# Optimization experiments

Hardware: AMD Instinct MI355X
Metric: run time of the kernel (lower is better)

Reference implementation:

```python
import jax, jax.numpy as jnp
import numpy as np


def setup_inputs() -> dict:
    key = jax.random.key(0)
    k1, k2, k3 = jax.random.split(key, 3)
    B, Na, Nb = 64, 8192, 8192
    phases_a = jax.random.normal(k1, (B, Na), dtype=jnp.float32)
    phases_b = jax.random.normal(k2, (B, Nb), dtype=jnp.float32)
    # Binary coupled-pair indicator mask (N_a, N_b)
    coupling_mask = jax.random.randint(k3, (Na, Nb), 0, 2, dtype=jnp.int32)
    return {"phases_a": phases_a, "phases_b": phases_b, "coupling_mask": coupling_mask}


def reference(phases_a, phases_b, coupling_mask):
    """Masked phase-locking value (PLV) between two oscillator banks.

    Mathematically identical to |sum_ij M_ij * exp(i*(a_i - b_j))| / sum(M),
    but computed via trig identities + matmul instead of materializing the
    O(B*Na*Nb) complex tensor:
      real = sum_ij M_ij (cos a_i cos b_j + sin a_i sin b_j)
      imag = sum_ij M_ij (sin a_i cos b_j - cos a_i sin b_j)
    """
    ca, sa = jnp.cos(phases_a), jnp.sin(phases_a)   # (B, Na)
    cb, sb = jnp.cos(phases_b), jnp.sin(phases_b)   # (B, Nb)
    M = coupling_mask.astype(ca.dtype)              # (Na, Nb)
    caM = ca @ M                                    # (B, Nb)
    saM = sa @ M                                    # (B, Nb)
    real = jnp.sum(caM * cb + saM * sb, axis=-1)    # (B,)
    imag = jnp.sum(saM * cb - caM * sb, axis=-1)    # (B,)
    n_pairs = jnp.maximum(M.sum(), jnp.asarray(1.0, ca.dtype))
    return jnp.sqrt(real * real + imag * imag) / n_pairs
```

## Files before the change

kernel.cpp:

```cpp
#include <hip/hip_runtime.h>
#include <hip/hip_bf16.h>

#define NA 8192
#define NB 8192
#define NBATCH 64
#define NC 128
#define BM 128
#define WM 32
#define SPLITK 8
#define KCHUNK (NB / SPLITK)

#define XT_BYTES (NC * NB * 2)
#define CTR_OFF  XT_BYTES
#define PPART_OFF (XT_BYTES + 4096)

typedef __bf16 bf16x8 __attribute__((ext_vector_type(8)));
typedef float  f32x4  __attribute__((ext_vector_type(4)));

__global__ __launch_bounds__(256) void prep_b_kernel(
    const float* __restrict__ pb, __hip_bfloat16* __restrict__ Xt)
{
    int tid = blockIdx.x * 256 + threadIdx.x;
    int b = tid >> 13;
    int j = tid & (NB - 1);
    float ph = pb[tid];
    float s, c;
    __sincosf(ph, &s, &c);
    Xt[(size_t)(2 * b) * NB + j]     = __float2bfloat16(c);
    Xt[(size_t)(2 * b + 1) * NB + j] = __float2bfloat16(s);
}

__global__ __launch_bounds__(256, 2) void gemm_kernel(
    const int* __restrict__ mask, const __hip_bfloat16* __restrict__ Xtg,
    float* __restrict__ Ppart, int* __restrict__ count)
{
    const int tid  = threadIdx.x;
    const int wave = tid >> 6;
    const int lane = tid & 63;
    const int quad = lane >> 4;
    const int m    = lane & 15;
    const int itile = blockIdx.x;
    const int kc    = blockIdx.y;
    const int k0    = kc * KCHUNK;

    const int rowbase = itile * BM + wave * WM;
    const ushort* xt = reinterpret_cast<const ushort*>(Xtg);

    f32x4 acc[2][8];
#pragma unroll
    for (int f = 0; f < 2; ++f)
#pragma unroll
        for (int t = 0; t < 8; ++t)
            acc[f][t] = (f32x4){0.f, 0.f, 0.f, 0.f};

    int cnt = 0;

    for (int kk = k0; kk < k0 + KCHUNK; kk += 32) {
        const int kq = kk + quad * 8;

        bf16x8 a[2];
#pragma unroll
        for (int f = 0; f < 2; ++f) {
            const int4* p = reinterpret_cast<const int4*>(
                mask + (size_t)(rowbase + f * 16 + m) * NB + kq);
            int4 r0 = p[0];
            int4 r1 = p[1];
            cnt += r0.x + r0.y + r0.z + r0.w + r1.x + r1.y + r1.z + r1.w;
            uint4 u;
            u.x = (r0.x ? 0x3F80u : 0u) | (r0.y ? 0x3F800000u : 0u);
            u.y = (r0.z ? 0x3F80u : 0u) | (r0.w ? 0x3F800000u : 0u);
            u.z = (r1.x ? 0x3F80u : 0u) | (r1.y ? 0x3F800000u : 0u);
            u.w = (r1.z ? 0x3F80u : 0u) | (r1.w ? 0x3F800000u : 0u);
            a[f] = __builtin_bit_cast(bf16x8, u);
        }

#pragma unroll
        for (int t = 0; t < 8; ++t) {
            const bf16x8 bfrag = *reinterpret_cast<const bf16x8*>(
                xt + (size_t)(t * 16 + m) * NB + kq);
            acc[0][t] = __builtin_amdgcn_mfma_f32_16x16x32_bf16(a[0], bfrag, acc[0][t], 0, 0, 0);
            acc[1][t] = __builtin_amdgcn_mfma_f32_16x16x32_bf16(a[1], bfrag, acc[1][t], 0, 0, 0);
        }
    }

    float* pout = Ppart + (size_t)kc * NA * NC;
#pragma unroll
    for (int f = 0; f < 2; ++f)
#pragma unroll
        for (int t = 0; t < 8; ++t)
#pragma unroll
            for (int r = 0; r < 4; ++r) {
                int row = rowbase + f * 16 + quad * 4 + r;
                int col = t * 16 + m;
                pout[(size_t)row * NC + col] = acc[f][t][r];
            }

#pragma unroll
    for (int off = 32; off > 0; off >>= 1) cnt += __shfl_down(cnt, off);
    if (lane == 0) atomicAdd(count, cnt);
}

__global__ __launch_bounds__(256) void reduce_kernel(
    const float* __restrict__ pa, const float* __restrict__ Ppart,
    float* __restrict__ realg, float* __restrict__ imagg)
{
    const int t = threadIdx.x;
    const int c = t & 127;
    const int half = t >> 7;
    const int b = c >> 1;
    const int odd = c & 1;
    const int i0 = blockIdx.x * 32;

    float pacc = 0.f, qacc = 0.f;
    for (int i = i0 + half; i < i0 + 32; i += 2) {
        float v = 0.f;
#pragma unroll
        for (int kc = 0; kc < SPLITK; ++kc)
            v += Ppart[(size_t)kc * NA * NC + (size_t)i * NC + c];
        float ph = pa[b * NA + i];
        float sn, cs;
        __sincosf(ph, &sn, &cs);
        float yc = odd ? sn : cs;
        float yo = odd ? cs : sn;
        pacc += yc * v;
        qacc += odd ? -(yo * v) : (yo * v);
    }

    __shared__ float red[2][256];
    red[0][t] = pacc;
    red[1][t] = qacc;
    __syncthreads();
    if (t < 128) {
        red[0][t] = red[0][t] + red[0][t + 128];
        red[1][t] = red[1][t] + red[1][t + 128];
    }
    __syncthreads();
    if (t < 64) {
        float real = red[0][2 * t] + red[0][2 * t + 1];
        float imag = red[1][2 * t] + red[1][2 * t + 1];
        atomicAdd(&realg[t], real);
        atomicAdd(&imagg[t], imag);
    }
}

__global__ void finalize_kernel(const float* __restrict__ realg,
                                const float* __restrict__ imagg,
                                const int* __restrict__ count,
                                float* __restrict__ out)
{
    int t = threadIdx.x;
    if (t < NBATCH) {
        float r = realg[t], im = imagg[t];
        float n = fmaxf((float)(*count), 1.0f);
        out[t] = sqrtf(r * r + im * im) / n;
    }
}

extern "C" void kernel_launch(void* const* d_in, const int* in_sizes, int n_in,
                              void* d_out, int out_size, void* d_ws, size_t ws_size,
                              hipStream_t stream) {
    const float* pa   = (const float*)d_in[0];
    const float* pb   = (const float*)d_in[1];
    const int*   mask = (const int*)d_in[2];
    float* out = (float*)d_out;

    char* ws = (char*)d_ws;
    __hip_bfloat16* Xt = (__hip_bfloat16*)ws;
    float* realg = (float*)(ws + CTR_OFF);
    float* imagg = realg + 64;
    int*   count = (int*)(ws + CTR_OFF + 512);
    float* Ppart = (float*)(ws + PPART_OFF);

    hipMemsetAsync(ws + CTR_OFF, 0, 4096, stream);

    prep_b_kernel<<<(NBATCH * NB) / 256, 256, 0, stream>>>(pb, Xt);

    dim3 g(NA / BM, SPLITK);
    gemm_kernel<<<g, 256, 0, stream>>>(mask, Xt, Ppart, count);

    reduce_kernel<<<NA / 32, 256, 0, stream>>>(pa, Ppart, realg, imagg);

    finalize_kernel<<<1, 64, 0, stream>>>(realg, imagg, count, out);
}
```

Measured before the change: 431.9 us.

## Compress int32 mask to bitmask before GEMM and permute B columns to match

```diff
diff --git a/kernel.cpp b/kernel.cpp
--- a/kernel.cpp
+++ b/kernel.cpp
@@ -9,30 +9,86 @@
 #define WM 32
 #define SPLITK 8
 #define KCHUNK (NB / SPLITK)
-
-#define XT_BYTES (NC * NB * 2)
-#define CTR_OFF  XT_BYTES
-#define PPART_OFF (XT_BYTES + 4096)
+#define NBW (NB / 32)
+
+#define XT_BYTES   (NC * NB * 2)
+#define BITS_OFF   XT_BYTES
+#define BITS_BYTES (NA * (NB / 8))
+#define CTR_OFF    (BITS_OFF + BITS_BYTES)
+#define PPART_OFF  (CTR_OFF + 4096)
 
 typedef __bf16 bf16x8 __attribute__((ext_vector_type(8)));
 typedef float  f32x4  __attribute__((ext_vector_type(4)));
 
+
+__global__ __launch_bounds__(256) void compress_kernel(
+    const int* __restrict__ mask, unsigned int* __restrict__ bits,
+    int* __restrict__ count)
+{
+    const int lane   = threadIdx.x & 63;
+    const int gwave  = (blockIdx.x * 256 + threadIdx.x) >> 6;
+    const int nwaves = (gridDim.x * 256) >> 6;
+
+    int cnt = 0;
+    const int total_iters = NA * (NB / 512);
+    for (int it = gwave; it < total_iters; it += nwaves) {
+        const int r  = it >> 4;
+        const int j0 = (it & 15) << 9;
+        const int4* p = reinterpret_cast<const int4*>(mask + (size_t)r * NB + j0);
+        int4 v0 = p[lane];
+        int4 v1 = p[lane + 64];
+
+        unsigned long long b0 = __ballot(v0.x != 0);
+        unsigned long long b1 = __ballot(v0.y != 0);
+        unsigned long long b2 = __ballot(v0.z != 0);
+        unsigned long long b3 = __ballot(v0.w != 0);
+        unsigned long long b4 = __ballot(v1.x != 0);
+        unsigned long long b5 = __ballot(v1.y != 0);
+        unsigned long long b6 = __ballot(v1.z != 0);
+        unsigned long long b7 = __ballot(v1.w != 0);
+
+        cnt += __builtin_popcountll(b0) + __builtin_popcountll(b1)
+             + __builtin_popcountll(b2) + __builtin_popcountll(b3)
+             + __builtin_popcountll(b4) + __builtin_popcountll(b5)
+             + __builtin_popcountll(b6) + __builtin_popcountll(b7);
+
+        if (lane == 0) {
+            uint4* o = reinterpret_cast<uint4*>(bits + (size_t)r * NBW + (j0 >> 5));
+            o[0] = (uint4){(unsigned)b0, (unsigned)(b0 >> 32), (unsigned)b1, (unsigned)(b1 >> 32)};
+            o[1] = (uint4){(unsigned)b2, (unsigned)(b2 >> 32), (unsigned)b3, (unsigned)(b3 >> 32)};
+            o[2] = (uint4){(unsigned)b4, (unsigned)(b4 >> 32), (unsigned)b5, (unsigned)(b5 >> 32)};
+            o[3] = (uint4){(unsigned)b6, (unsigned)(b6 >> 32), (unsigned)b7, (unsigned)(b7 >> 32)};
+        }
+    }
+    if (lane == 0) atomicAdd(count, cnt);
+}
+
 __global__ __launch_bounds__(256) void prep_b_kernel(
     const float* __restrict__ pb, __hip_bfloat16* __restrict__ Xt)
 {
     int tid = blockIdx.x * 256 + threadIdx.x;
-    int b = tid >> 13;
-    int j = tid & (NB - 1);
-    float ph = pb[tid];
+    int b  = tid >> 13;
+    int kp = tid & (NB - 1);
+    int j  = (kp & ~255) | ((kp & 63) << 2) | ((kp >> 6) & 3);
+    float ph = pb[(size_t)b * NB + j];
     float s, c;
     __sincosf(ph, &s, &c);
-    Xt[(size_t)(2 * b) * NB + j]     = __float2bfloat16(c);
-    Xt[(size_t)(2 * b + 1) * NB + j] = __float2bfloat16(s);
+    Xt[(size_t)(2 * b) * NB + kp]     = __float2bfloat16(c);
+    Xt[(size_t)(2 * b + 1) * NB + kp] = __float2bfloat16(s);
+}
+
+__device__ inline bf16x8 expand8(unsigned int byte) {
+    uint4 u;
+    u.x = ((((byte >> 1) & 1u) << 16) | (byte & 1u))          * 0x3F80u;
+    u.y = ((((byte >> 3) & 1u) << 16) | ((byte >> 2) & 1u))   * 0x3F80u;
+    u.z = ((((byte >> 5) & 1u) << 16) | ((byte >> 4) & 1u))   * 0x3F80u;
+    u.w = ((((byte >> 7) & 1u) << 16) | ((byte >> 6) & 1u))   * 0x3F80u;
+    return __builtin_bit_cast(bf16x8, u);
 }
 
 __global__ __launch_bounds__(256, 2) void gemm_kernel(
-    const int* __restrict__ mask, const __hip_bfloat16* __restrict__ Xtg,
-    float* __restrict__ Ppart, int* __restrict__ count)
+    const unsigned int* __restrict__ bits, const __hip_bfloat16* __restrict__ Xtg,
+    float* __restrict__ Ppart)
 {
     const int tid  = threadIdx.x;
     const int wave = tid >> 6;
@@ -45,6 +101,7 @@
 
     const int rowbase = itile * BM + wave * WM;
     const ushort* xt = reinterpret_cast<const ushort*>(Xtg);
+    const int qsh = quad * 8;
 
     f32x4 acc[2][8];
 #pragma unroll
@@ -53,33 +110,24 @@
         for (int t = 0; t < 8; ++t)
             acc[f][t] = (f32x4){0.f, 0.f, 0.f, 0.f};
 
-    int cnt = 0;
+    const unsigned int* w0p = bits + (size_t)(rowbase + m) * NBW;
+    const unsigned int* w1p = bits + (size_t)(rowbase + 16 + m) * NBW;
 
     for (int kk = k0; kk < k0 + KCHUNK; kk += 32) {
-        const int kq = kk + quad * 8;
-
-        bf16x8 a[2];
-#pragma unroll
-        for (int f = 0; f < 2; ++f) {
-            const int4* p = reinterpret_cast<const int4*>(
-                mask + (size_t)(rowbase + f * 16 + m) * NB + kq);
-            int4 r0 = p[0];
-            int4 r1 = p[1];
-            cnt += r0.x + r0.y + r0.z + r0.w + r1.x + r1.y + r1.z + r1.w;
-            uint4 u;
-            u.x = (r0.x ? 0x3F80u : 0u) | (r0.y ? 0x3F800000u : 0u);
-            u.y = (r0.z ? 0x3F80u : 0u) | (r0.w ? 0x3F800000u : 0u);
-            u.z = (r1.x ? 0x3F80u : 0u) | (r1.y ? 0x3F800000u : 0u);
-            u.w = (r1.z ? 0x3F80u : 0u) | (r1.w ? 0x3F800000u : 0u);
-            a[f] = __builtin_bit_cast(bf16x8, u);
-        }
+        const int wi = kk >> 5;
+        unsigned int w0 = w0p[wi];
+        unsigned int w1 = w1p[wi];
+        const int kq = kk + qsh;
+
+        bf16x8 a0 = expand8((w0 >> qsh) & 0xFFu);
+        bf16x8 a1 = expand8((w1 >> qsh) & 0xFFu);
 
 #pragma unroll
         for (int t = 0; t < 8; ++t) {
             const bf16x8 bfrag = *reinterpret_cast<const bf16x8*>(
                 xt + (size_t)(t * 16 + m) * NB + kq);
-            acc[0][t] = __builtin_amdgcn_mfma_f32_16x16x32_bf16(a[0], bfrag, acc[0][t], 0, 0, 0);
-            acc[1][t] = __builtin_amdgcn_mfma_f32_16x16x32_bf16(a[1], bfrag, acc[1][t], 0, 0, 0);
+            acc[0][t] = __builtin_amdgcn_mfma_f32_16x16x32_bf16(a0, bfrag, acc[0][t], 0, 0, 0);
+            acc[1][t] = __builtin_amdgcn_mfma_f32_16x16x32_bf16(a1, bfrag, acc[1][t], 0, 0, 0);
         }
     }
 
@@ -94,10 +142,6 @@
                 int col = t * 16 + m;
                 pout[(size_t)row * NC + col] = acc[f][t][r];
             }
-
-#pragma unroll
-    for (int off = 32; off > 0; off >>= 1) cnt += __shfl_down(cnt, off);
-    if (lane == 0) atomicAdd(count, cnt);
 }
 
 __global__ __launch_bounds__(256) void reduce_kernel(
@@ -117,7 +161,7 @@
 #pragma unroll
         for (int kc = 0; kc < SPLITK; ++kc)
             v += Ppart[(size_t)kc * NA * NC + (size_t)i * NC + c];
-        float ph = pa[b * NA + i];
+        float ph = pa[(size_t)b * NA + i];
         float sn, cs;
         __sincosf(ph, &sn, &cs);
         float yc = odd ? sn : cs;
@@ -166,6 +210,7 @@
 
     char* ws = (char*)d_ws;
     __hip_bfloat16* Xt = (__hip_bfloat16*)ws;
+    unsigned int* bitsw = (unsigned int*)(ws + BITS_OFF);
     float* realg = (float*)(ws + CTR_OFF);
     float* imagg = realg + 64;
     int*   count = (int*)(ws + CTR_OFF + 512);
@@ -173,10 +218,12 @@
 
     hipMemsetAsync(ws + CTR_OFF, 0, 4096, stream);
 
+    compress_kernel<<<2048, 256, 0, stream>>>(mask, bitsw, count);
+
     prep_b_kernel<<<(NBATCH * NB) / 256, 256, 0, stream>>>(pb, Xt);
 
     dim3 g(NA / BM, SPLITK);
-    gemm_kernel<<<g, 256, 0, stream>>>(mask, Xt, Ppart, count);
+    gemm_kernel<<<g, 256, 0, stream>>>(bitsw, Xt, Ppart);
 
     reduce_kernel<<<NA / 32, 256, 0, stream>>>(pa, Ppart, realg, imagg);
 
```

Result: slower. 501.4 us (+16.1%).
